# Kernel optimization log

Measured on AMD Instinct MI355X. Metric: run time of the kernel, lower is better.

Reference implementation:

```python
import jax, jax.numpy as jnp
import numpy as np

DIM = 1024
NUM_HEADS = 16
HEAD_DIM = DIM // NUM_HEADS
SCALE = HEAD_DIM ** -0.5


def setup_inputs() -> dict:
    key = jax.random.key(0)
    ks = jax.random.split(key, 5)
    x = jax.random.normal(ks[0], (8, 1024, DIM), dtype=jnp.float32)
    # nn.Linear default init ~ U(-1/sqrt(fan_in), 1/sqrt(fan_in)); use scaled normals
    w_qkv = jax.random.normal(ks[1], (DIM, 3 * DIM), dtype=jnp.float32) * (DIM ** -0.5)
    b_qkv = jax.random.normal(ks[2], (3 * DIM,), dtype=jnp.float32) * 0.02
    w_proj = jax.random.normal(ks[3], (DIM, DIM), dtype=jnp.float32) * (DIM ** -0.5)
    b_proj = jax.random.normal(ks[4], (DIM,), dtype=jnp.float32) * 0.02
    return {"x": x, "w_qkv": w_qkv, "b_qkv": b_qkv, "w_proj": w_proj, "b_proj": b_proj}


def reference(x, w_qkv, b_qkv, w_proj, b_proj):
    B, N, D = x.shape
    qkv = x @ w_qkv + b_qkv                       # [B, N, 3D]
    qkv = qkv.reshape(B, N, 3, NUM_HEADS, HEAD_DIM)
    qkv = jnp.transpose(qkv, (2, 0, 3, 1, 4))     # [3, B, H, N, hd]
    q, k, v = qkv[0], qkv[1], qkv[2]
    attn = jnp.einsum('bhqd,bhkd->bhqk', q, k) * SCALE
    attn = jax.nn.softmax(attn, axis=-1)
    out = jnp.einsum('bhqk,bhkd->bhqd', attn, v)  # [B, H, N, hd]
    out = jnp.transpose(out, (0, 2, 1, 3)).reshape(B, N, D)
    out = out @ w_proj + b_proj
    return out
```

## Files before the change

### kernel.cpp

```cpp
#include <hip/hip_runtime.h>
#include <stdint.h>


typedef short bf16x8 __attribute__((ext_vector_type(8)));
typedef float f32x4 __attribute__((ext_vector_type(4)));
typedef uint32_t u32x2 __attribute__((ext_vector_type(2)));

__device__ __forceinline__ short f32_bf16(float f) {
  uint32_t u = __builtin_bit_cast(uint32_t, f);
  u += 0x7FFFu + ((u >> 16) & 1u);
  return (short)(u >> 16);
}

__device__ __forceinline__ float exp2_fast(float x) {
  float r; asm("v_exp_f32 %0, %1" : "=v"(r) : "v"(x)); return r;
}

__device__ __forceinline__ uint32_t cvt_pk_bf16(float lo, float hi) {
  uint32_t r;
  asm("v_cvt_pk_bf16_f32 %0, %1, %2" : "=v"(r) : "v"(lo), "v"(hi));
  return r;
}

__device__ __forceinline__ void gload_lds16(const void* g, void* l) {
  __builtin_amdgcn_global_load_lds(
      (const __attribute__((address_space(1))) uint32_t*)g,
      (__attribute__((address_space(3))) uint32_t*)l, 16, 0, 0);
}

__global__ __launch_bounds__(256) void convert_x_kernel(
    const float* __restrict__ x, short* __restrict__ xb) {
  int i = blockIdx.x * 256 + threadIdx.x;
  const float4 f0 = ((const float4*)x)[i * 2];
  const float4 f1 = ((const float4*)x)[i * 2 + 1];
  bf16x8 o;
  o[0] = f32_bf16(f0.x); o[1] = f32_bf16(f0.y);
  o[2] = f32_bf16(f0.z); o[3] = f32_bf16(f0.w);
  o[4] = f32_bf16(f1.x); o[5] = f32_bf16(f1.y);
  o[6] = f32_bf16(f1.z); o[7] = f32_bf16(f1.w);
  ((bf16x8*)xb)[i] = o;
}

__global__ __launch_bounds__(256) void transpose_w_kernel(
    const float* __restrict__ w, short* __restrict__ wt, int N) {
  __shared__ float tile[64][65];
  const int n0 = blockIdx.x * 64, k0 = blockIdx.y * 64;
  const int tr = threadIdx.x >> 6, tc = threadIdx.x & 63;
#pragma unroll
  for (int i = 0; i < 16; ++i) {
    int k = tr + i * 4;
    tile[k][tc] = w[(size_t)(k0 + k) * N + n0 + tc];
  }
  __syncthreads();
#pragma unroll
  for (int i = 0; i < 16; ++i) {
    int a = tr + i * 4;
    wt[(size_t)(n0 + a) * 1024 + k0 + tc] = f32_bf16(tile[tc][a]);
  }
}

template <int EPI>
__global__ __launch_bounds__(256, 2) void gemm4_kernel(
    const short* __restrict__ A, const short* __restrict__ Bt,
    const float* __restrict__ bias, short* __restrict__ Qb,
    short* __restrict__ Kb, short* __restrict__ Vt, float* __restrict__ out,
    int NTN) {
  __shared__ short Asm[2][128 * 64];
  __shared__ short Bsm[2][128 * 64];

  const int tid = threadIdx.x;
  const int lane = tid & 63;
  const int w = tid >> 6;
  const int wr = w >> 1, wc = w & 1;
  const int c = lane & 15, g = lane >> 4;

  const int nwg = gridDim.x;
  const int wg = (blockIdx.x & 7) * (nwg >> 3) + (blockIdx.x >> 3);
  const int tm = wg / NTN, tn = wg % NTN;
  const int m0 = tm * 128, n0 = tn * 128;

  f32x4 acc[4][4] = {};

  auto stage = [&](int dbuf, int kk0) {
#pragma unroll
    for (int ci = 0; ci < 4; ++ci) {
      const int p = ci * 256 + tid;
      const int r = p >> 3, s = p & 7;
      gload_lds16(A + (size_t)(m0 + r) * 1024 + kk0 + ((s ^ (r & 7)) * 8),
                  &Asm[dbuf][p * 8]);
    }
#pragma unroll
    for (int ci = 0; ci < 4; ++ci) {
      const int p = ci * 256 + tid;
      const int r = p >> 3, s = p & 7;
      gload_lds16(Bt + (size_t)(n0 + r) * 1024 + kk0 + ((s ^ (r & 7)) * 8),
                  &Bsm[dbuf][p * 8]);
    }
  };

  stage(0, 0);

  for (int t = 0; t < 16; ++t) {
    const int buf = t & 1;
    if (t < 15) {
      stage(buf ^ 1, (t + 1) * 64);
      asm volatile("s_waitcnt vmcnt(8)" ::: "memory");
    } else {
      asm volatile("s_waitcnt vmcnt(0)" ::: "memory");
    }
    __builtin_amdgcn_s_barrier();
    __builtin_amdgcn_sched_barrier(0);

    bf16x8 bfr[4][2];
#pragma unroll
    for (int jn = 0; jn < 4; ++jn) {
      const int S = wc * 64 + jn * 16 + c;
#pragma unroll
      for (int kk = 0; kk < 2; ++kk)
        bfr[jn][kk] = *(const bf16x8*)&Bsm[buf][S * 64 + (((kk * 4 + g) ^ (c & 7)) * 8)];
    }
#pragma unroll
    for (int mq = 0; mq < 2; ++mq) {
      bf16x8 af[2][2];
#pragma unroll
      for (int mm = 0; mm < 2; ++mm) {
        const int R = wr * 64 + (mq * 2 + mm) * 16 + c;
#pragma unroll
        for (int kk = 0; kk < 2; ++kk)
          af[mm][kk] = *(const bf16x8*)&Asm[buf][R * 64 + (((kk * 4 + g) ^ (c & 7)) * 8)];
      }
      asm volatile("s_waitcnt lgkmcnt(0)" ::: "memory");
      __builtin_amdgcn_sched_barrier(0);
      __builtin_amdgcn_s_setprio(1);
#pragma unroll
      for (int mm = 0; mm < 2; ++mm)
#pragma unroll
        for (int jn = 0; jn < 4; ++jn)
#pragma unroll
          for (int kk = 0; kk < 2; ++kk)
            acc[mq * 2 + mm][jn] = __builtin_amdgcn_mfma_f32_16x16x32_bf16(
                af[mm][kk], bfr[jn][kk], acc[mq * 2 + mm][jn], 0, 0, 0);
      __builtin_amdgcn_s_setprio(0);
    }
    __builtin_amdgcn_s_barrier();
    __builtin_amdgcn_sched_barrier(0);
  }

#pragma unroll
  for (int mm = 0; mm < 4; ++mm) {
    const int i_base = m0 + wr * 64 + mm * 16 + 4 * g;
#pragma unroll
    for (int nn = 0; nn < 4; ++nn) {
      const int j = n0 + wc * 64 + nn * 16 + c;
      const float bj = bias[j];
      if (EPI == 0) {
        const int three = j >> 10, rem = j & 1023, h = rem >> 6, d = rem & 63;
        const float sc = (three == 1) ? 0.18033688f : 1.0f;
#pragma unroll
        for (int r = 0; r < 4; ++r) {
          const int i = i_base + r;
          const int bb = i >> 10, nnq = i & 1023;
          const int bh = bb * 16 + h;
          const short bv = f32_bf16((acc[mm][nn][r] + bj) * sc);
          if (three == 0)
            Qb[(size_t)(bh * 1024 + nnq) * 64 + d] = bv;
          else if (three == 1)
            Kb[(size_t)(bh * 1024 + nnq) * 64 + d] = bv;
          else
            Vt[(size_t)(bh * 64 + d) * 1024 + nnq] = bv;
        }
      } else {
#pragma unroll
        for (int r = 0; r < 4; ++r)
          out[(size_t)(i_base + r) * 1024 + j] = acc[mm][nn][r] + bj;
      }
    }
  }
}

__global__ __launch_bounds__(256, 2) void attn_kernel(
    const short* __restrict__ Qb, const short* __restrict__ Kb,
    const short* __restrict__ Vt, short* __restrict__ Ao) {
  __shared__ __align__(16) char smem[25600];
  short* Kf = (short*)smem;
  short* Vf = (short*)(smem + 8192);
  short* Pl = (short*)(smem + 16384);

  const int tid = threadIdx.x, lane = tid & 63, w = tid >> 6;
  const int c = lane & 15, g = lane >> 4;
  const int bh = blockIdx.x >> 3, qb = blockIdx.x & 7;
  const int bb = bh >> 4, h = bh & 15;
  const int q0 = qb * 128 + w * 32;

  bf16x8 qf[2][2];
#pragma unroll
  for (int m = 0; m < 2; ++m)
#pragma unroll
    for (int ks = 0; ks < 2; ++ks)
      qf[m][ks] = *(const bf16x8*)(Qb + (size_t)(bh * 1024 + q0 + m * 16 + c) * 64 + ks * 32 + 8 * g);

  f32x4 o[2][4] = {};
  float mrun[2] = {-3.0e38f, -3.0e38f};
  float lrun[2] = {0.f, 0.f};

  const int row_r = tid >> 2, seg = tid & 3;
  const short* kp = Kb + (size_t)(bh * 1024 + row_r) * 64 + seg * 16;
  const short* vp = Vt + (size_t)(bh * 64 + row_r) * 1024 + seg * 16;
  short *kdst0, *kdst1, *vdst0, *vdst1;
  {
    const int d0a = seg * 16, d0b = seg * 16 + 8;
    const int pa = (row_r >> 4) * 2 + (d0a >> 5);
    const int pb = (row_r >> 4) * 2 + (d0b >> 5);
    const int sa = (row_r & 15) + 16 * ((d0a & 31) >> 3);
    const int sb = (row_r & 15) + 16 * ((d0b & 31) >> 3);
    kdst0 = &Kf[(pa * 64 + sa) * 8]; kdst1 = &Kf[(pb * 64 + sb) * 8];
    vdst0 = &Vf[(pa * 64 + sa) * 8]; vdst1 = &Vf[(pb * 64 + sb) * 8];
  }

  uint32_t* plw = (uint32_t*)(Pl + w * 1152);
  const short* plr = Pl + w * 1152;

  auto compute = [&]() {
#pragma unroll
    for (int m = 0; m < 2; ++m) {
      f32x4 s[4];
#pragma unroll
      for (int kt = 0; kt < 4; ++kt) {
        f32x4 sa = {};
#pragma unroll
        for (int ks = 0; ks < 2; ++ks) {
          bf16x8 kb = *(const bf16x8*)&Kf[((kt * 2 + ks) * 64 + lane) * 8];
          sa = __builtin_amdgcn_mfma_f32_16x16x32_bf16(kb, qf[m][ks], sa, 0, 0, 0);
        }
        s[kt] = sa;
      }
      float vmax = s[0][0];
#pragma unroll
      for (int kt = 0; kt < 4; ++kt)
#pragma unroll
        for (int r = 0; r < 4; ++r) vmax = fmaxf(vmax, s[kt][r]);
      vmax = fmaxf(vmax, __shfl_xor(vmax, 16));
      vmax = fmaxf(vmax, __shfl_xor(vmax, 32));
      if (!__all(vmax <= mrun[m] + 8.0f)) {
        float mnew = fmaxf(mrun[m], vmax);
        float al = exp2_fast(mrun[m] - mnew);
        lrun[m] *= al;
#pragma unroll
        for (int dt = 0; dt < 4; ++dt) o[m][dt] *= al;
        mrun[m] = mnew;
      }
      float rs = 0.f;
#pragma unroll
      for (int kt = 0; kt < 4; ++kt) {
        float p0 = exp2_fast(s[kt][0] - mrun[m]);
        float p1 = exp2_fast(s[kt][1] - mrun[m]);
        float p2 = exp2_fast(s[kt][2] - mrun[m]);
        float p3 = exp2_fast(s[kt][3] - mrun[m]);
        rs += (p0 + p1) + (p2 + p3);
        u32x2 pk;
        pk[0] = cvt_pk_bf16(p0, p1);
        pk[1] = cvt_pk_bf16(p2, p3);
        *(u32x2*)&plw[c * 36 + kt * 8 + 2 * g] = pk;
      }
      rs += __shfl_xor(rs, 16);
      rs += __shfl_xor(rs, 32);
      lrun[m] += rs;
#pragma unroll
      for (int kk = 0; kk < 2; ++kk) {
        bf16x8 pb = *(const bf16x8*)(plr + c * 72 + kk * 32 + 8 * g);
#pragma unroll
        for (int dt = 0; dt < 4; ++dt) {
          bf16x8 vb = *(const bf16x8*)&Vf[((dt * 2 + kk) * 64 + lane) * 8];
          o[m][dt] = __builtin_amdgcn_mfma_f32_16x16x32_bf16(vb, pb, o[m][dt], 0, 0, 0);
        }
      }
    }
  };

  bf16x8 ka0, ka1, va0, va1, kc0, kc1, vc0, vc1;
  ka0 = *(const bf16x8*)(kp);     ka1 = *(const bf16x8*)(kp + 8);
  va0 = *(const bf16x8*)(vp);     va1 = *(const bf16x8*)(vp + 8);

  for (int t = 0; t < 16; t += 2) {
    __syncthreads();
    *(bf16x8*)kdst0 = ka0; *(bf16x8*)kdst1 = ka1;
    *(bf16x8*)vdst0 = va0; *(bf16x8*)vdst1 = va1;
    {
      const short* kpt = kp + (size_t)(t + 1) * 4096;
      const short* vpt = vp + (t + 1) * 64;
      kc0 = *(const bf16x8*)(kpt); kc1 = *(const bf16x8*)(kpt + 8);
      vc0 = *(const bf16x8*)(vpt); vc1 = *(const bf16x8*)(vpt + 8);
    }
    __syncthreads();
    compute();
    __syncthreads();
    *(bf16x8*)kdst0 = kc0; *(bf16x8*)kdst1 = kc1;
    *(bf16x8*)vdst0 = vc0; *(bf16x8*)vdst1 = vc1;
    if (t + 2 < 16) {
      const short* kpt = kp + (size_t)(t + 2) * 4096;
      const short* vpt = vp + (t + 2) * 64;
      ka0 = *(const bf16x8*)(kpt); ka1 = *(const bf16x8*)(kpt + 8);
      va0 = *(const bf16x8*)(vpt); va1 = *(const bf16x8*)(vpt + 8);
    }
    __syncthreads();
    compute();
  }

  __syncthreads();
  float* Osc = (float*)smem + w * (16 * 68);
  const int qrow = lane >> 2, dseg = (lane & 3) << 4;
#pragma unroll
  for (int m = 0; m < 2; ++m) {
    const float inv = 1.0f / lrun[m];
#pragma unroll
    for (int dt = 0; dt < 4; ++dt)
#pragma unroll
      for (int r = 0; r < 4; ++r)
        Osc[c * 68 + dt * 16 + 4 * g + r] = o[m][dt][r] * inv;
#pragma unroll
    for (int j = 0; j < 2; ++j) {
      f32x4 a0 = *(f32x4*)&Osc[qrow * 68 + dseg + j * 8];
      f32x4 a1 = *(f32x4*)&Osc[qrow * 68 + dseg + j * 8 + 4];
      bf16x8 ob;
      ob[0] = f32_bf16(a0[0]); ob[1] = f32_bf16(a0[1]);
      ob[2] = f32_bf16(a0[2]); ob[3] = f32_bf16(a0[3]);
      ob[4] = f32_bf16(a1[0]); ob[5] = f32_bf16(a1[1]);
      ob[6] = f32_bf16(a1[2]); ob[7] = f32_bf16(a1[3]);
      *(bf16x8*)(Ao + (size_t)(bb * 1024 + q0 + m * 16 + qrow) * 1024 + h * 64 + dseg + j * 8) = ob;
    }
    __syncthreads();
  }
}

extern "C" void kernel_launch(void* const* d_in, const int* in_sizes, int n_in,
                              void* d_out, int out_size, void* d_ws, size_t ws_size,
                              hipStream_t stream) {
  const float* x = (const float*)d_in[0];
  const float* w_qkv = (const float*)d_in[1];
  const float* b_qkv = (const float*)d_in[2];
  const float* w_proj = (const float*)d_in[3];
  const float* b_proj = (const float*)d_in[4];
  float* out = (float*)d_out;

  char* ws = (char*)d_ws;
  const size_t XB_OFF = 0;
  const size_t WQKVT_OFF = 16777216;
  const size_t WPROJT_OFF = WQKVT_OFF + 6291456;
  const size_t Q_OFF = WPROJT_OFF + 2097152;
  const size_t K_OFF = Q_OFF + 16777216;
  const size_t VT_OFF = K_OFF + 16777216;
  short* xb = (short*)(ws + XB_OFF);
  short* wqkvT = (short*)(ws + WQKVT_OFF);
  short* wprojT = (short*)(ws + WPROJT_OFF);
  short* Qb = (short*)(ws + Q_OFF);
  short* Kb = (short*)(ws + K_OFF);
  short* Vt = (short*)(ws + VT_OFF);
  short* attn_o = xb;

  convert_x_kernel<<<dim3(4096), dim3(256), 0, stream>>>(x, xb);
  transpose_w_kernel<<<dim3(48, 16), dim3(256), 0, stream>>>(w_qkv, wqkvT, 3072);
  transpose_w_kernel<<<dim3(16, 16), dim3(256), 0, stream>>>(w_proj, wprojT, 1024);
  gemm4_kernel<0><<<dim3(1536), dim3(256), 0, stream>>>(
      xb, wqkvT, b_qkv, Qb, Kb, Vt, nullptr, 24);
  attn_kernel<<<dim3(1024), dim3(256), 0, stream>>>(Qb, Kb, Vt, attn_o);
  gemm4_kernel<1><<<dim3(512), dim3(256), 0, stream>>>(
      attn_o, wprojT, b_proj, nullptr, nullptr, nullptr, out, 8);
}
```

Baseline: 273.3 us.

## Merge prep kernels into one launch and single-buffer GEMM LDS for occupancy

Folds the x conversion and both weight transposes into one prep kernel, dispatched by block index, which saves two kernel launches. The GEMM drops LDS double buffering: each K step loads its tile, waits for all loads and then computes. This halves LDS per block, and launch bounds rise to 4 blocks per CU. The aim is to hide memory latency with more resident blocks instead of software prefetch, at the cost of exposing load latency inside each block. Four blocks of 256 threads may also be hard to fit given the 64 accumulator registers per thread.

```diff
diff --git a/kernel.cpp b/kernel.cpp
--- a/kernel.cpp
+++ b/kernel.cpp
@@ -28,24 +28,33 @@
       (__attribute__((address_space(3))) uint32_t*)l, 16, 0, 0);
 }
 
-__global__ __launch_bounds__(256) void convert_x_kernel(
-    const float* __restrict__ x, short* __restrict__ xb) {
-  int i = blockIdx.x * 256 + threadIdx.x;
-  const float4 f0 = ((const float4*)x)[i * 2];
-  const float4 f1 = ((const float4*)x)[i * 2 + 1];
-  bf16x8 o;
-  o[0] = f32_bf16(f0.x); o[1] = f32_bf16(f0.y);
-  o[2] = f32_bf16(f0.z); o[3] = f32_bf16(f0.w);
-  o[4] = f32_bf16(f1.x); o[5] = f32_bf16(f1.y);
-  o[6] = f32_bf16(f1.z); o[7] = f32_bf16(f1.w);
-  ((bf16x8*)xb)[i] = o;
-}
-
-__global__ __launch_bounds__(256) void transpose_w_kernel(
-    const float* __restrict__ w, short* __restrict__ wt, int N) {
+__global__ __launch_bounds__(256) void prep_kernel(
+    const float* __restrict__ x, short* __restrict__ xb,
+    const float* __restrict__ w_qkv, short* __restrict__ wqkvT,
+    const float* __restrict__ w_proj, short* __restrict__ wprojT) {
   __shared__ float tile[64][65];
-  const int n0 = blockIdx.x * 64, k0 = blockIdx.y * 64;
-  const int tr = threadIdx.x >> 6, tc = threadIdx.x & 63;
+  const int bx = blockIdx.x, tid = threadIdx.x;
+  if (bx < 4096) {
+    const int i = bx * 256 + tid;
+    const float4 f0 = ((const float4*)x)[i * 2];
+    const float4 f1 = ((const float4*)x)[i * 2 + 1];
+    bf16x8 o;
+    o[0] = f32_bf16(f0.x); o[1] = f32_bf16(f0.y);
+    o[2] = f32_bf16(f0.z); o[3] = f32_bf16(f0.w);
+    o[4] = f32_bf16(f1.x); o[5] = f32_bf16(f1.y);
+    o[6] = f32_bf16(f1.z); o[7] = f32_bf16(f1.w);
+    ((bf16x8*)xb)[i] = o;
+    return;
+  }
+  const float* w; short* wt; int N, n0, k0;
+  if (bx < 4864) {
+    const int b = bx - 4096;
+    w = w_qkv; wt = wqkvT; N = 3072; n0 = (b % 48) * 64; k0 = (b / 48) * 64;
+  } else {
+    const int b = bx - 4864;
+    w = w_proj; wt = wprojT; N = 1024; n0 = (b % 16) * 64; k0 = (b / 16) * 64;
+  }
+  const int tr = tid >> 6, tc = tid & 63;
 #pragma unroll
   for (int i = 0; i < 16; ++i) {
     int k = tr + i * 4;
@@ -60,13 +69,13 @@
 }
 
 template <int EPI>
-__global__ __launch_bounds__(256, 2) void gemm4_kernel(
+__global__ __launch_bounds__(256, 4) void gemm4_kernel(
     const short* __restrict__ A, const short* __restrict__ Bt,
     const float* __restrict__ bias, short* __restrict__ Qb,
     short* __restrict__ Kb, short* __restrict__ Vt, float* __restrict__ out,
     int NTN) {
-  __shared__ short Asm[2][128 * 64];
-  __shared__ short Bsm[2][128 * 64];
+  __shared__ short Asm[128 * 64];
+  __shared__ short Bsm[128 * 64];
 
   const int tid = threadIdx.x;
   const int lane = tid & 63;
@@ -81,33 +90,26 @@
 
   f32x4 acc[4][4] = {};
 
-  auto stage = [&](int dbuf, int kk0) {
+  auto stage = [&](int kk0) {
 #pragma unroll
     for (int ci = 0; ci < 4; ++ci) {
       const int p = ci * 256 + tid;
       const int r = p >> 3, s = p & 7;
       gload_lds16(A + (size_t)(m0 + r) * 1024 + kk0 + ((s ^ (r & 7)) * 8),
-                  &Asm[dbuf][p * 8]);
+                  &Asm[p * 8]);
     }
 #pragma unroll
     for (int ci = 0; ci < 4; ++ci) {
       const int p = ci * 256 + tid;
       const int r = p >> 3, s = p & 7;
       gload_lds16(Bt + (size_t)(n0 + r) * 1024 + kk0 + ((s ^ (r & 7)) * 8),
-                  &Bsm[dbuf][p * 8]);
+                  &Bsm[p * 8]);
     }
   };
 
-  stage(0, 0);
-
   for (int t = 0; t < 16; ++t) {
-    const int buf = t & 1;
-    if (t < 15) {
-      stage(buf ^ 1, (t + 1) * 64);
-      asm volatile("s_waitcnt vmcnt(8)" ::: "memory");
-    } else {
-      asm volatile("s_waitcnt vmcnt(0)" ::: "memory");
-    }
+    stage(t * 64);
+    asm volatile("s_waitcnt vmcnt(0)" ::: "memory");
     __builtin_amdgcn_s_barrier();
     __builtin_amdgcn_sched_barrier(0);
 
@@ -117,7 +119,7 @@
       const int S = wc * 64 + jn * 16 + c;
 #pragma unroll
       for (int kk = 0; kk < 2; ++kk)
-        bfr[jn][kk] = *(const bf16x8*)&Bsm[buf][S * 64 + (((kk * 4 + g) ^ (c & 7)) * 8)];
+        bfr[jn][kk] = *(const bf16x8*)&Bsm[S * 64 + (((kk * 4 + g) ^ (c & 7)) * 8)];
     }
 #pragma unroll
     for (int mq = 0; mq < 2; ++mq) {
@@ -127,7 +129,7 @@
         const int R = wr * 64 + (mq * 2 + mm) * 16 + c;
 #pragma unroll
         for (int kk = 0; kk < 2; ++kk)
-          af[mm][kk] = *(const bf16x8*)&Asm[buf][R * 64 + (((kk * 4 + g) ^ (c & 7)) * 8)];
+          af[mm][kk] = *(const bf16x8*)&Asm[R * 64 + (((kk * 4 + g) ^ (c & 7)) * 8)];
       }
       asm volatile("s_waitcnt lgkmcnt(0)" ::: "memory");
       __builtin_amdgcn_sched_barrier(0);
@@ -357,9 +359,8 @@
   short* Vt = (short*)(ws + VT_OFF);
   short* attn_o = xb;
 
-  convert_x_kernel<<<dim3(4096), dim3(256), 0, stream>>>(x, xb);
-  transpose_w_kernel<<<dim3(48, 16), dim3(256), 0, stream>>>(w_qkv, wqkvT, 3072);
-  transpose_w_kernel<<<dim3(16, 16), dim3(256), 0, stream>>>(w_proj, wprojT, 1024);
+  prep_kernel<<<dim3(5120), dim3(256), 0, stream>>>(
+      x, xb, w_qkv, wqkvT, w_proj, wprojT);
   gemm4_kernel<0><<<dim3(1536), dim3(256), 0, stream>>>(
       xb, wqkvT, b_qkv, Qb, Kb, Vt, nullptr, 24);
   attn_kernel<<<dim3(1024), dim3(256), 0, stream>>>(Qb, Kb, Vt, attn_o);
```

New measurement: 303.0 us. 1.11x slower.
